# Kernel tuning notes

Measured on AMD Instinct MI355X. Metric: run time of the kernel, lower is better.

Reference implementation:

```python
import jax, jax.numpy as jnp
import numpy as np

H, C = 4, 32            # heads, per-head out channels -> H*C = 128
NEG = jnp.float32(-1e9) # stand-in for -inf mask (keeps grads finite)
NUM_LOC = 15            # self.num_locations hardcoded to 15


def _tconv(x, src, dst, ea, Wq, bq, Wk, bk, Wv, bv, We, Ws, bs, Wb):
    # PyG TransformerConv(beta=True, concat=True, edge_dim=1)
    N = x.shape[0]
    q = (x @ Wq + bq).reshape(N, H, C)
    k = (x @ Wk + bk).reshape(N, H, C)
    v = (x @ Wv + bv).reshape(N, H, C)
    e = (ea @ We).reshape(-1, H, C)  # edge embedding [E,H,C]
    kj = k[src] + e
    alpha = jnp.einsum('ehc,ehc->eh', q[dst], kj) / jnp.sqrt(jnp.float32(C))
    # scatter-softmax over incoming edges of each dst node
    amax = jax.ops.segment_max(alpha, dst, num_segments=N)
    ex = jnp.exp(alpha - amax[dst])
    den = jax.ops.segment_sum(ex, dst, num_segments=N)
    w = ex / (den[dst] + 1e-16)
    out = jax.ops.segment_sum((v[src] + e) * w[..., None], dst, num_segments=N).reshape(N, H * C)
    xr = x @ Ws + bs  # lin_skip
    beta = jax.nn.sigmoid(jnp.concatenate([out, xr, out - xr], axis=-1) @ Wb)  # [N,1]
    return beta * xr + (1.0 - beta) * out


def _bn(x, g, b):
    # BatchNorm1d in training mode (batch statistics, biased var)
    m = x.mean(0)
    v = ((x - m) ** 2).mean(0)
    return (x - m) * jax.lax.rsqrt(v + 1e-5) * g + b


def _forward_core(fa, edge_index, active_mask):
    (node_type, requests, latency,
     c0_Wq, c0_bq, c0_Wk, c0_bk, c0_Wv, c0_bv, c0_We, c0_Ws, c0_bs, c0_Wb,
     t0_W, t0_b, bn0_g, bn0_b,
     cs_Wq, cs_bq, cs_Wk, cs_bk, cs_Wv, cs_bv, cs_We, cs_Ws, cs_bs, cs_Wb,
     ts_W, ts_b, bns_g, bns_b,
     emb_W1, emb_b1, emb_W2, emb_b2, emb_W3, emb_b3,
     rem_W, rem_b, add_W, add_b) = fa
    src, dst = edge_index[0], edge_index[1]
    ea = latency[:, None]                      # edge_attr [E,1]
    x = jnp.stack([node_type, requests], axis=1)  # [N,2]
    # NetworkGraphEmbeddingConstructor: conv1 + 4 stacked conv/linear/bn blocks
    x = _tconv(x, src, dst, ea, c0_Wq, c0_bq, c0_Wk, c0_bk, c0_Wv, c0_bv, c0_We, c0_Ws, c0_bs, c0_Wb)
    x = _bn(jax.nn.relu(x @ t0_W + t0_b), bn0_g, bn0_b)
    for i in range(4):
        x = _tconv(x, src, dst, ea, cs_Wq[i], cs_bq[i], cs_Wk[i], cs_bk[i], cs_Wv[i], cs_bv[i], cs_We[i], cs_Ws[i], cs_bs[i], cs_Wb[i])
        x = _bn(jax.nn.relu(x @ ts_W[i] + ts_b[i]), bns_g[i], bns_b[i])
    # embedding_transformation MLP
    x = jax.nn.relu(x @ emb_W1 + emb_b1)
    x = jax.nn.relu(x @ emb_W2 + emb_b2)
    x = x @ emb_W3 + emb_b3                    # [N,64]
    # sampling head (batch_index=None branch)
    N = x.shape[0]
    maskf = jnp.where(active_mask == 1, jnp.float32(0.0), NEG)
    loc = jnp.arange(N) < NUM_LOC
    remove_mask = jnp.where(loc, jnp.where(maskf == 0.0, NEG, jnp.float32(0.0)), maskf)
    logits1 = (x @ rem_W + rem_b)[:, 0] + remove_mask
    k1, k2 = jax.random.split(jax.random.key(42))
    a1 = jnp.argmax(logits1 + jax.random.gumbel(k1, (N,), logits1.dtype))  # Categorical sample
    mask2 = maskf.at[a1].set(0.0)
    t = jnp.tanh(x[a1] @ add_W + add_b)        # [64]
    logits2 = x @ t + mask2
    a2 = jnp.argmax(logits2 + jax.random.gumbel(k2, (N,), logits2.dtype))
    log_probs = jnp.stack([jax.nn.log_softmax(logits1)[a1], jax.nn.log_softmax(logits2)[a2]])
    return jnp.stack([logits1, logits2]), jnp.stack([a1, a2]), log_probs


def setup_inputs() -> dict:
    N, E = 50000, 400000
    F, HC, EMB, L = 2, 128, 32, 4
    key = jax.random.key(0)
    kit = iter(jax.random.split(key, 64))
    def w(shape, s=0.1):
        return jax.random.normal(next(kit), shape, jnp.float32) * s
    return {
        'node_type': w((N,), 1.0),
        'requests': jax.random.uniform(next(kit), (N,), jnp.float32),
        'latency': jax.random.uniform(next(kit), (E,), jnp.float32),
        'edge_index': jax.random.randint(next(kit), (2, E), 0, N, jnp.int32),
        'active_mask': jax.random.randint(next(kit), (N,), 0, 2, jnp.int32),
        'c0_Wq': w((F, HC)), 'c0_bq': w((HC,)),
        'c0_Wk': w((F, HC)), 'c0_bk': w((HC,)),
        'c0_Wv': w((F, HC)), 'c0_bv': w((HC,)),
        'c0_We': w((1, HC)),
        'c0_Ws': w((F, HC)), 'c0_bs': w((HC,)),
        'c0_Wb': w((3 * HC, 1)),
        't0_W': w((HC, EMB)), 't0_b': w((EMB,)),
        'bn0_g': jnp.ones((EMB,), jnp.float32), 'bn0_b': jnp.zeros((EMB,), jnp.float32),
        'cs_Wq': w((L, EMB, HC)), 'cs_bq': w((L, HC)),
        'cs_Wk': w((L, EMB, HC)), 'cs_bk': w((L, HC)),
        'cs_Wv': w((L, EMB, HC)), 'cs_bv': w((L, HC)),
        'cs_We': w((L, 1, HC)),
        'cs_Ws': w((L, EMB, HC)), 'cs_bs': w((L, HC)),
        'cs_Wb': w((L, 3 * HC, 1)),
        'ts_W': w((L, HC, EMB)), 'ts_b': w((L, EMB)),
        'bns_g': jnp.ones((L, EMB), jnp.float32), 'bns_b': jnp.zeros((L, EMB), jnp.float32),
        'emb_W1': w((EMB, 128)), 'emb_b1': w((128,)),
        'emb_W2': w((128, 64)), 'emb_b2': w((64,)),
        'emb_W3': w((64, 64)), 'emb_b3': w((64,)),
        'rem_W': w((64, 1)), 'rem_b': w((1,)),
        'add_W': w((64, 64)), 'add_b': w((64,)),
    }


def reference(node_type, requests, latency, edge_index, active_mask,
              c0_Wq, c0_bq, c0_Wk, c0_bk, c0_Wv, c0_bv, c0_We, c0_Ws, c0_bs, c0_Wb,
              t0_W, t0_b, bn0_g, bn0_b,
              cs_Wq, cs_bq, cs_Wk, cs_bk, cs_Wv, cs_bv, cs_We, cs_Ws, cs_bs, cs_Wb,
              ts_W, ts_b, bns_g, bns_b,
              emb_W1, emb_b1, emb_W2, emb_b2, emb_W3, emb_b3,
              rem_W, rem_b, add_W, add_b):
    fa = (node_type, requests, latency,
          c0_Wq, c0_bq, c0_Wk, c0_bk, c0_Wv, c0_bv, c0_We, c0_Ws, c0_bs, c0_Wb,
          t0_W, t0_b, bn0_g, bn0_b,
          cs_Wq, cs_bq, cs_Wk, cs_bk, cs_Wv, cs_bv, cs_We, cs_Ws, cs_bs, cs_Wb,
          ts_W, ts_b, bns_g, bns_b,
          emb_W1, emb_b1, emb_W2, emb_b2, emb_W3, emb_b3,
          rem_W, rem_b, add_W, add_b)
    return _forward_core(fa, edge_index, active_mask)
```

## Files before the change

### kernel.cpp

```cpp
#include <hip/hip_runtime.h>
#include <hip/hip_fp16.h>
#include <cstdint>
#include <math.h>

typedef _Float16 h2 __attribute__((ext_vector_type(2)));
typedef float f32x2 __attribute__((ext_vector_type(2)));

__device__ __forceinline__ h2 f2h2(float a, float b) {
    h2 r; r.x = (_Float16)a; r.y = (_Float16)b; return r;
}
__device__ __forceinline__ float fdot2f(h2 a, h2 b, float c) {
    return __builtin_amdgcn_fdot2(a, b, c, false);
}
__device__ __forceinline__ f32x2 bc2(float x) { f32x2 r; r.x = x; r.y = x; return r; }
__device__ __forceinline__ f32x2 cvt2(h2 v) {
    f32x2 r; r.x = (float)v.x; r.y = (float)v.y; return r;
}
__device__ __forceinline__ f32x2 mk2(float a, float b) { f32x2 r; r.x = a; r.y = b; return r; }

union f4h {
    float4 f;
    h2 h[4];
    __half2 u[4];
};

__device__ __forceinline__ uint32_t rotl32(uint32_t x, uint32_t n) {
    return (x << n) | (x >> (32u - n));
}

__device__ __forceinline__ void tf2x32(uint32_t k0, uint32_t k1,
                                       uint32_t x0, uint32_t x1,
                                       uint32_t& o0, uint32_t& o1) {
    uint32_t k2 = k0 ^ k1 ^ 0x1BD11BDAu;
    x0 += k0; x1 += k1;
    x0 += x1; x1 = rotl32(x1, 13); x1 ^= x0;
    x0 += x1; x1 = rotl32(x1, 15); x1 ^= x0;
    x0 += x1; x1 = rotl32(x1, 26); x1 ^= x0;
    x0 += x1; x1 = rotl32(x1, 6);  x1 ^= x0;
    x0 += k1; x1 += k2 + 1u;
    x0 += x1; x1 = rotl32(x1, 17); x1 ^= x0;
    x0 += x1; x1 = rotl32(x1, 29); x1 ^= x0;
    x0 += x1; x1 = rotl32(x1, 16); x1 ^= x0;
    x0 += x1; x1 = rotl32(x1, 24); x1 ^= x0;
    x0 += k2; x1 += k0 + 2u;
    x0 += x1; x1 = rotl32(x1, 13); x1 ^= x0;
    x0 += x1; x1 = rotl32(x1, 15); x1 ^= x0;
    x0 += x1; x1 = rotl32(x1, 26); x1 ^= x0;
    x0 += x1; x1 = rotl32(x1, 6);  x1 ^= x0;
    x0 += k0; x1 += k1 + 3u;
    x0 += x1; x1 = rotl32(x1, 17); x1 ^= x0;
    x0 += x1; x1 = rotl32(x1, 29); x1 ^= x0;
    x0 += x1; x1 = rotl32(x1, 16); x1 ^= x0;
    x0 += x1; x1 = rotl32(x1, 24); x1 ^= x0;
    x0 += k1; x1 += k2 + 4u;
    x0 += x1; x1 = rotl32(x1, 13); x1 ^= x0;
    x0 += x1; x1 = rotl32(x1, 15); x1 ^= x0;
    x0 += x1; x1 = rotl32(x1, 26); x1 ^= x0;
    x0 += x1; x1 = rotl32(x1, 6);  x1 ^= x0;
    x0 += k2; x1 += k0 + 5u;
    o0 = x0; o1 = x1;
}

__device__ float gumbel_at(int n, int which, int N) {
    uint32_t a0, a1, b0, b1;
    tf2x32(0u, 42u, 0u, 2u, a0, a1);
    tf2x32(0u, 42u, 1u, 3u, b0, b1);
    uint32_t gk0 = which ? a1 : a0;
    uint32_t gk1 = which ? b1 : b0;
    int half = N >> 1;
    uint32_t o0, o1, bits;
    if (n < half) { tf2x32(gk0, gk1, (uint32_t)n, (uint32_t)(n + half), o0, o1); bits = o0; }
    else          { tf2x32(gk0, gk1, (uint32_t)(n - half), (uint32_t)n, o0, o1); bits = o1; }
    float f = __uint_as_float((bits >> 9) | 0x3F800000u) - 1.0f;
    float u = fmaxf(1.17549435e-38f, f);
    return -logf(-logf(u));
}

__device__ __forceinline__ uint32_t fmono(float f) {
    uint32_t b = __float_as_uint(f);
    return (b & 0x80000000u) ? ~b : (b | 0x80000000u);
}
__device__ __forceinline__ float funmono(uint32_t u) {
    uint32_t b = (u & 0x80000000u) ? (u & 0x7FFFFFFFu) : ~u;
    return __uint_as_float(b);
}

__device__ __forceinline__ void lse_merge(float& m, float& s, float m2, float s2) {
    float M = fmaxf(m, m2);
    float a = (m == -INFINITY) ? 0.f : expf(m - M) * s;
    float b = (m2 == -INFINITY) ? 0.f : expf(m2 - M) * s2;
    m = M; s = a + b;
}

#define NEGF (-1e9f)
#define ATTNGRID 2048

__global__ void k_hist(const int* __restrict__ dstp, int* __restrict__ deg, int E) {
    int e = blockIdx.x * 256 + threadIdx.x;
    if (e < E) atomicAdd(&deg[dstp[e]], 1);
}

__global__ void k_scan1(const int* __restrict__ deg, int* __restrict__ bsum, int N) {
    __shared__ int s[256];
    int i = blockIdx.x * 256 + threadIdx.x;
    s[threadIdx.x] = (i < N) ? deg[i] : 0;
    __syncthreads();
    for (int st = 128; st > 0; st >>= 1) {
        if (threadIdx.x < st) s[threadIdx.x] += s[threadIdx.x + st];
        __syncthreads();
    }
    if (threadIdx.x == 0) bsum[blockIdx.x] = s[0];
}

__global__ void k_scan2(int* __restrict__ bsum, int nb) {
    __shared__ int s[256];
    int i = threadIdx.x;
    int v = (i < nb) ? bsum[i] : 0;
    s[i] = v;
    __syncthreads();
    for (int st = 1; st < 256; st <<= 1) {
        int t = (i >= st) ? s[i - st] : 0;
        __syncthreads();
        s[i] += t;
        __syncthreads();
    }
    if (i < nb) bsum[i] = s[i] - v;
}

__global__ void k_scan3(const int* __restrict__ deg, const int* __restrict__ bsum,
                        int* __restrict__ rowptr, int* __restrict__ cursor, int N) {
    __shared__ int s[256];
    int i = blockIdx.x * 256 + threadIdx.x;
    int v = (i < N) ? deg[i] : 0;
    s[threadIdx.x] = v;
    __syncthreads();
    for (int st = 1; st < 256; st <<= 1) {
        int t = (threadIdx.x >= st) ? s[threadIdx.x - st] : 0;
        __syncthreads();
        s[threadIdx.x] += t;
        __syncthreads();
    }
    int excl = s[threadIdx.x] - v + bsum[blockIdx.x];
    if (i < N) { rowptr[i] = excl; cursor[i] = excl; }
}

__global__ void k_fill(const int* __restrict__ dstp, const int* __restrict__ srcp,
                       const float* __restrict__ lat, int* __restrict__ cursor,
                       int2* __restrict__ srclat, int E) {
    int e = blockIdx.x * 256 + threadIdx.x;
    if (e < E) {
        int pos = atomicAdd(&cursor[dstp[e]], 1);
        srclat[pos] = make_int2(srcp[e], __float_as_int(lat[e]));
    }
}

__global__ __launch_bounds__(512, 4) void k_qkvr(
        const float* __restrict__ xin, const float* __restrict__ nt,
        const float* __restrict__ rq, int din, int N,
        const float* __restrict__ Wq, const float* __restrict__ bq,
        const float* __restrict__ Wk, const float* __restrict__ bk,
        const float* __restrict__ Wv, const float* __restrict__ bv,
        const float* __restrict__ Ws, const float* __restrict__ bs,
        const double* __restrict__ SUM, const double* __restrict__ SUMSQ,
        const float* __restrict__ bng, const float* __restrict__ bnb,
        int applyBN,
        __half* __restrict__ Q, __half* __restrict__ KV, __half* __restrict__ R) {
    __shared__ h2 w2[4][16 * 128];
    __shared__ float bias[4][128];
    __shared__ h2 xs2[32][17];
    __shared__ float sscale[32], sshift[32];
    int t = threadIdx.x;
    int dpCount = din >> 1;
    for (int i = t; i < dpCount * 128; i += 512) {
        int dp = i >> 7, j = i & 127;
        w2[0][i] = f2h2(Wq[(size_t)(2 * dp) * 128 + j], Wq[(size_t)(2 * dp + 1) * 128 + j]);
        w2[1][i] = f2h2(Wk[(size_t)(2 * dp) * 128 + j], Wk[(size_t)(2 * dp + 1) * 128 + j]);
        w2[2][i] = f2h2(Wv[(size_t)(2 * dp) * 128 + j], Wv[(size_t)(2 * dp + 1) * 128 + j]);
        w2[3][i] = f2h2(Ws[(size_t)(2 * dp) * 128 + j], Ws[(size_t)(2 * dp + 1) * 128 + j]);
    }
    if (t < 128) {
        bias[0][t] = bq[t]; bias[1][t] = bk[t]; bias[2][t] = bv[t]; bias[3][t] = bs[t];
    }
    if (t < 32) {
        if (applyBN) {
            double m = SUM[t] / N;
            double v = SUMSQ[t] / N - m * m;
            float inv = rsqrtf((float)v + 1e-5f);
            float sc = inv * bng[t];
            sscale[t] = sc;
            sshift[t] = bnb[t] - (float)m * sc;
        } else {
            sscale[t] = 1.f; sshift[t] = 0.f;
        }
    }
    int quad = t & 31;
    int sub = t >> 5;
    int dpsh = (din == 32) ? 4 : 0;
    int tiles = (N + 31) >> 5;
    for (int tile = blockIdx.x; tile < tiles; tile += gridDim.x) {
        int base = tile << 5;
        __syncthreads();
        for (int i = t; i < 32 * dpCount; i += 512) {
            int nl = i >> dpsh, dp = i & (dpCount - 1);
            int nn = base + nl;
            float x0 = 0.f, x1 = 0.f;
            if (nn < N) {
                if (din == 2) { x0 = nt[nn]; x1 = rq[nn]; }
                else {
                    x0 = xin[(size_t)nn * din + 2 * dp];
                    x1 = xin[(size_t)nn * din + 2 * dp + 1];
                }
            }
            x0 = x0 * sscale[2 * dp] + sshift[2 * dp];
            x1 = x1 * sscale[2 * dp + 1] + sshift[2 * dp + 1];
            xs2[nl][dp] = f2h2(x0, x1);
        }
        __syncthreads();
        float acc[4][2][4];
#pragma unroll
        for (int m = 0; m < 4; ++m)
#pragma unroll
            for (int k = 0; k < 2; ++k)
#pragma unroll
                for (int c = 0; c < 4; ++c) acc[m][k][c] = bias[m][quad * 4 + c];
        for (int dp = 0; dp < dpCount; ++dp) {
            h2 xv0 = xs2[sub * 2 + 0][dp];
            h2 xv1 = xs2[sub * 2 + 1][dp];
#pragma unroll
            for (int m = 0; m < 4; ++m) {
                const h2* wp = &w2[m][dp * 128 + quad * 4];
                h2 wa = wp[0], wb = wp[1], wc = wp[2], wd = wp[3];
                acc[m][0][0] = fdot2f(xv0, wa, acc[m][0][0]);
                acc[m][0][1] = fdot2f(xv0, wb, acc[m][0][1]);
                acc[m][0][2] = fdot2f(xv0, wc, acc[m][0][2]);
                acc[m][0][3] = fdot2f(xv0, wd, acc[m][0][3]);
                acc[m][1][0] = fdot2f(xv1, wa, acc[m][1][0]);
                acc[m][1][1] = fdot2f(xv1, wb, acc[m][1][1]);
                acc[m][1][2] = fdot2f(xv1, wc, acc[m][1][2]);
                acc[m][1][3] = fdot2f(xv1, wd, acc[m][1][3]);
            }
        }
#pragma unroll
        for (int k = 0; k < 2; ++k) {
            int n = base + sub * 2 + k;
            if (n < N) {
                *(__half2*)&Q[(size_t)n * 128 + quad * 4 + 0] =
                    __floats2half2_rn(acc[0][k][0], acc[0][k][1]);
                *(__half2*)&Q[(size_t)n * 128 + quad * 4 + 2] =
                    __floats2half2_rn(acc[0][k][2], acc[0][k][3]);
                *(__half2*)&KV[(size_t)n * 256 + quad * 4 + 0] =
                    __floats2half2_rn(acc[1][k][0], acc[1][k][1]);
                *(__half2*)&KV[(size_t)n * 256 + quad * 4 + 2] =
                    __floats2half2_rn(acc[1][k][2], acc[1][k][3]);
                *(__half2*)&KV[(size_t)n * 256 + 128 + quad * 4 + 0] =
                    __floats2half2_rn(acc[2][k][0], acc[2][k][1]);
                *(__half2*)&KV[(size_t)n * 256 + 128 + quad * 4 + 2] =
                    __floats2half2_rn(acc[2][k][2], acc[2][k][3]);
                *(__half2*)&R[(size_t)n * 128 + quad * 4 + 0] =
                    __floats2half2_rn(acc[3][k][0], acc[3][k][1]);
                *(__half2*)&R[(size_t)n * 128 + quad * 4 + 2] =
                    __floats2half2_rn(acc[3][k][2], acc[3][k][3]);
            }
        }
    }
}

__global__ __launch_bounds__(256) void k_attn(
        const int2* __restrict__ srclat,
        const __half* __restrict__ Q, const __half* __restrict__ KV,
        const float* __restrict__ We,
        const __half* __restrict__ R, const float* __restrict__ Wb,
        const int* __restrict__ rowptr, const int* __restrict__ deg,
        __half* __restrict__ A, int N) {
    __shared__ float weL[128], wboL[128], wbrL[128];
    int t = threadIdx.x;
    if (t < 128) {
        float w0 = Wb[t], w1 = Wb[128 + t], w2v = Wb[256 + t];
        weL[t] = We[t];
        wboL[t] = w0 + w2v;
        wbrL[t] = w1 - w2v;
    }
    __syncthreads();

    int wvid = t >> 6;
    int l64 = t & 63;
    int slot = (l64 >> 4) & 1;
    int nsub = l64 >> 5;
    int lane = l64 & 15;
    const f32x2* wep = (const f32x2*)&weL[lane * 8];
    const f32x2* bop = (const f32x2*)&wboL[lane * 8];
    const f32x2* brp = (const f32x2*)&wbrL[lane * 8];
    h2 weh0, weh1, weh2, weh3;
    {
        f32x2 wa = wep[0], wb = wep[1], wc = wep[2], wd = wep[3];
        weh0 = f2h2(wa.x, wa.y); weh1 = f2h2(wb.x, wb.y);
        weh2 = f2h2(wc.x, wc.y); weh3 = f2h2(wd.x, wd.y);
    }
    const float4 f4z = make_float4(0.f, 0.f, 0.f, 0.f);

    int T = gridDim.x * 4;
    int T2 = T * 2;
    int base0 = (blockIdx.x * 4 + wvid) * 2;

    f4h qh, rh, k0, v0;
    int start = 0, d = 0; float l0 = 0.f;
    f4h pq, pr, pk, pv;
    float pl = 0.f;
    int s1 = 0, d1 = 0;
    int2 psl1 = make_int2(0, 0);
    int s2 = 0, d2 = 0;
    qh.f = f4z; rh.f = f4z; k0.f = f4z; v0.f = f4z;
    pq.f = f4z; pr.f = f4z; pk.f = f4z; pv.f = f4z;

    {
        int n0l = base0 + nsub;
        if (n0l < N) {
            start = rowptr[n0l]; d = deg[n0l];
            qh.f = *(const float4*)(Q + (size_t)n0l * 128 + lane * 8);
            rh.f = *(const float4*)(R + (size_t)n0l * 128 + lane * 8);
            if (slot < d) {
                int2 sl = srclat[start + slot];
                l0 = __int_as_float(sl.y);
                k0.f = *(const float4*)(KV + (size_t)sl.x * 256 + lane * 8);
                v0.f = *(const float4*)(KV + (size_t)sl.x * 256 + 128 + lane * 8);
            }
            int n1l = n0l + T2;
            if (n1l < N) {
                s1 = rowptr[n1l]; d1 = deg[n1l];
                if (slot < d1) psl1 = srclat[s1 + slot];
            }
            int n2l = n0l + 2 * T2;
            if (n2l < N) { s2 = rowptr[n2l]; d2 = deg[n2l]; }
        }
    }

    for (int nb = base0; nb < N; nb += T2) {
        int n = nb + nsub;
        int n1 = n + T2, n2 = n + 2 * T2, n3 = n + 3 * T2;
        int s3 = 0, d3 = 0;
        if (n3 < N) { s3 = rowptr[n3]; d3 = deg[n3]; }
        int2 psl2 = make_int2(0, 0);
        if (n2 < N && slot < d2) psl2 = srclat[s2 + slot];
        if (n1 < N) {
            pq.f = *(const float4*)(Q + (size_t)n1 * 128 + lane * 8);
            pr.f = *(const float4*)(R + (size_t)n1 * 128 + lane * 8);
            if (slot < d1) {
                pl = __int_as_float(psl1.y);
                pk.f = *(const float4*)(KV + (size_t)psl1.x * 256 + lane * 8);
                pv.f = *(const float4*)(KV + (size_t)psl1.x * 256 + 128 + lane * 8);
            }
        }

        float qwe = fdot2f(qh.h[0], weh0, fdot2f(qh.h[1], weh1,
                    fdot2f(qh.h[2], weh2, fdot2f(qh.h[3], weh3, 0.f))));
        qwe += __shfl_xor(qwe, 1); qwe += __shfl_xor(qwe, 2);

        float m = -INFINITY, den = 0.f, plsum = 0.f;
        f32x2 A0 = bc2(0.f), A1 = bc2(0.f), A2 = bc2(0.f), A3 = bc2(0.f);

        int idx = slot;
        bool have = idx < d;
        while (have) {
            int idx2 = idx + 2;
            bool have2 = idx2 < d;
            float l1 = 0.f;
            f4h k1, v1;
            if (have2) {
                int2 sl = srclat[start + idx2];
                l1 = __int_as_float(sl.y);
                k1.f = *(const float4*)(KV + (size_t)sl.x * 256 + lane * 8);
                v1.f = *(const float4*)(KV + (size_t)sl.x * 256 + 128 + lane * 8);
            }

            float t0 = fdot2f(qh.h[0], k0.h[0], fdot2f(qh.h[1], k0.h[1],
                       fdot2f(qh.h[2], k0.h[2], fdot2f(qh.h[3], k0.h[3], 0.f))));
            t0 += __shfl_xor(t0, 1); t0 += __shfl_xor(t0, 2);
            float alpha = fmaf(l0, qwe, t0) * 0.17677669529663687f;

            float mn = fmaxf(m, alpha);
            float sc = __expf(m - mn);
            float p = __expf(alpha - mn);
            f32x2 sc2 = bc2(sc), p2 = bc2(p);
            A0 = A0 * sc2 + p2 * cvt2(v0.h[0]);
            A1 = A1 * sc2 + p2 * cvt2(v0.h[1]);
            A2 = A2 * sc2 + p2 * cvt2(v0.h[2]);
            A3 = A3 * sc2 + p2 * cvt2(v0.h[3]);
            plsum = plsum * sc + p * l0;
            den = fmaf(den, sc, p);
            m = mn;

            idx = idx2; l0 = l1;
            k0.f = k1.f; v0.f = v1.f;
            have = have2;
        }

        {
            float mo = __shfl_xor(m, 16);
            float mn = fmaxf(m, mo);
            float sc = (m == -INFINITY) ? 0.f : __expf(m - mn);
            f32x2 sc2 = bc2(sc);
            A0 *= sc2; A1 *= sc2; A2 *= sc2; A3 *= sc2;
            den *= sc; plsum *= sc;
            A0 += mk2(__shfl_xor(A0.x, 16), __shfl_xor(A0.y, 16));
            A1 += mk2(__shfl_xor(A1.x, 16), __shfl_xor(A1.y, 16));
            A2 += mk2(__shfl_xor(A2.x, 16), __shfl_xor(A2.y, 16));
            A3 += mk2(__shfl_xor(A3.x, 16), __shfl_xor(A3.y, 16));
            den += __shfl_xor(den, 16); plsum += __shfl_xor(plsum, 16);
            m = mn;
        }

        float inv = 1.f / (den + 1e-16f);
        f32x2 inv2 = bc2(inv), pls2 = bc2(plsum);
        f32x2 O0 = (A0 + pls2 * wep[0]) * inv2;
        f32x2 O1 = (A1 + pls2 * wep[1]) * inv2;
        f32x2 O2 = (A2 + pls2 * wep[2]) * inv2;
        f32x2 O3 = (A3 + pls2 * wep[3]) * inv2;

        f32x2 R0 = cvt2(rh.h[0]), R1 = cvt2(rh.h[1]);
        f32x2 R2 = cvt2(rh.h[2]), R3 = cvt2(rh.h[3]);
        f32x2 G = O0 * bop[0];
        G += R0 * brp[0];
        G += O1 * bop[1]; G += R1 * brp[1];
        G += O2 * bop[2]; G += R2 * brp[2];
        G += O3 * bop[3]; G += R3 * brp[3];
        float g = G.x + G.y;
        g += __shfl_xor(g, 1); g += __shfl_xor(g, 2);
        g += __shfl_xor(g, 4); g += __shfl_xor(g, 8);
        float beta = 1.0f / (1.0f + __expf(-g));

        if ((l64 & 16) == 0 && n < N) {
            f32x2 bb = bc2(beta), ib = bc2(1.0f - beta);
            f32x2 W0 = bb * R0 + ib * O0;
            f32x2 W1 = bb * R1 + ib * O1;
            f32x2 W2 = bb * R2 + ib * O2;
            f32x2 W3 = bb * R3 + ib * O3;
            *(__half2*)&A[(size_t)n * 128 + lane * 8 + 0] = __floats2half2_rn(W0.x, W0.y);
            *(__half2*)&A[(size_t)n * 128 + lane * 8 + 2] = __floats2half2_rn(W1.x, W1.y);
            *(__half2*)&A[(size_t)n * 128 + lane * 8 + 4] = __floats2half2_rn(W2.x, W2.y);
            *(__half2*)&A[(size_t)n * 128 + lane * 8 + 6] = __floats2half2_rn(W3.x, W3.y);
        }

        qh.f = pq.f; rh.f = pr.f; k0.f = pk.f; v0.f = pv.f; l0 = pl;
        start = s1; d = d1;
        s1 = s2; d1 = d2; s2 = s3; d2 = d3;
        psl1 = psl2;
    }
}

__global__ __launch_bounds__(256) void k_linstats(
        const __half* __restrict__ A, const float* __restrict__ tW,
        const float* __restrict__ tb, float* __restrict__ H32,
        double* __restrict__ partials, int N) {
    __shared__ h2 w2l[64 * 32];
    __shared__ float bias[32];
    __shared__ h2 xsT[64][66];
    __shared__ double sp1[4][8][4], sp2[4][8][4];
    int t = threadIdx.x;
    for (int i = t; i < 64 * 32; i += 256) {
        int dp = i >> 5, j = i & 31;
        w2l[i] = f2h2(tW[(size_t)(2 * dp) * 32 + j], tW[(size_t)(2 * dp + 1) * 32 + j]);
    }
    if (t < 32) bias[t] = tb[t];
    int quad = t & 7;
    int sub = t >> 3;
    int base = blockIdx.x << 6;

    __syncthreads();
#pragma unroll
    for (int k = 0; k < 4; ++k) {
        int i = t + 256 * k;
        int nl = i >> 4, g8 = i & 15;
        int n = base + nl;
        h2 hv[4];
        if (n < N) {
            const h2* ap = (const h2*)(A + (size_t)n * 128 + g8 * 8);
            hv[0] = ap[0]; hv[1] = ap[1]; hv[2] = ap[2]; hv[3] = ap[3];
        } else {
            h2 z; z.x = (_Float16)0.f; z.y = (_Float16)0.f;
            hv[0] = z; hv[1] = z; hv[2] = z; hv[3] = z;
        }
        xsT[g8 * 4 + 0][nl] = hv[0];
        xsT[g8 * 4 + 1][nl] = hv[1];
        xsT[g8 * 4 + 2][nl] = hv[2];
        xsT[g8 * 4 + 3][nl] = hv[3];
    }
    __syncthreads();

    float acc[2][4];
#pragma unroll
    for (int k = 0; k < 2; ++k)
#pragma unroll
        for (int c = 0; c < 4; ++c) acc[k][c] = bias[quad * 4 + c];
    for (int dp = 0; dp < 64; ++dp) {
        h2 x0 = xsT[dp][sub * 2 + 0];
        h2 x1 = xsT[dp][sub * 2 + 1];
        const h2* wp = &w2l[dp * 32 + quad * 4];
        h2 wa = wp[0], wb = wp[1], wc = wp[2], wd = wp[3];
        acc[0][0] = fdot2f(x0, wa, acc[0][0]);
        acc[0][1] = fdot2f(x0, wb, acc[0][1]);
        acc[0][2] = fdot2f(x0, wc, acc[0][2]);
        acc[0][3] = fdot2f(x0, wd, acc[0][3]);
        acc[1][0] = fdot2f(x1, wa, acc[1][0]);
        acc[1][1] = fdot2f(x1, wb, acc[1][1]);
        acc[1][2] = fdot2f(x1, wc, acc[1][2]);
        acc[1][3] = fdot2f(x1, wd, acc[1][3]);
    }
    double s1[4] = {0, 0, 0, 0}, s2[4] = {0, 0, 0, 0};
#pragma unroll
    for (int k = 0; k < 2; ++k) {
        int n = base + sub * 2 + k;
        if (n < N) {
            float4 yv;
            yv.x = fmaxf(acc[k][0], 0.f); yv.y = fmaxf(acc[k][1], 0.f);
            yv.z = fmaxf(acc[k][2], 0.f); yv.w = fmaxf(acc[k][3], 0.f);
            *(float4*)&H32[(size_t)n * 32 + quad * 4] = yv;
            s1[0] += yv.x; s1[1] += yv.y; s1[2] += yv.z; s1[3] += yv.w;
            s2[0] += (double)yv.x * yv.x; s2[1] += (double)yv.y * yv.y;
            s2[2] += (double)yv.z * yv.z; s2[3] += (double)yv.w * yv.w;
        }
    }
#pragma unroll
    for (int c = 0; c < 4; ++c) {
        s1[c] += __shfl_xor(s1[c], 8);  s2[c] += __shfl_xor(s2[c], 8);
        s1[c] += __shfl_xor(s1[c], 16); s2[c] += __shfl_xor(s2[c], 16);
        s1[c] += __shfl_xor(s1[c], 32); s2[c] += __shfl_xor(s2[c], 32);
    }
    __syncthreads();
    int wave = t >> 6;
    if ((t & 63) < 8) {
#pragma unroll
        for (int c = 0; c < 4; ++c) { sp1[wave][quad][c] = s1[c]; sp2[wave][quad][c] = s2[c]; }
    }
    __syncthreads();
    if (t < 32) {
        int q = t >> 2, c = t & 3;
        double a1 = 0, a2 = 0;
#pragma unroll
        for (int wv = 0; wv < 4; ++wv) { a1 += sp1[wv][q][c]; a2 += sp2[wv][q][c]; }
        partials[(size_t)blockIdx.x * 64 + t] = a1;
        partials[(size_t)blockIdx.x * 64 + 32 + t] = a2;
    }
}

__global__ void k_statred(const double* __restrict__ partials,
                          double* __restrict__ SUM, double* __restrict__ SUMSQ,
                          int nblocks) {
    __shared__ double s[256];
    int col = blockIdx.x;
    double a = 0;
    for (int b = threadIdx.x; b < nblocks; b += 256)
        a += partials[(size_t)b * 64 + col];
    s[threadIdx.x] = a;
    __syncthreads();
    for (int st = 128; st > 0; st >>= 1) {
        if (threadIdx.x < st) s[threadIdx.x] += s[threadIdx.x + st];
        __syncthreads();
    }
    if (threadIdx.x == 0) {
        if (col < 32) SUM[col] = s[0];
        else SUMSQ[col - 32] = s[0];
    }
}

__global__ __launch_bounds__(256) void k_mlp12(
        const float* __restrict__ H32,
        const double* __restrict__ SUM, const double* __restrict__ SUMSQ,
        const float* __restrict__ bng, const float* __restrict__ bnb,
        const float* __restrict__ W1, const float* __restrict__ b1,
        const float* __restrict__ W2, const float* __restrict__ b2,
        float* __restrict__ Y2, unsigned int* __restrict__ smallbuf, int N) {
    __shared__ float w1[32 * 128];
    __shared__ float sb1[128];
    __shared__ float sscale[32], sshift[32];
    __shared__ float w2f[128 * 64];
    __shared__ float sb2[64];
    __shared__ float xs[16][36];
    __shared__ float y1[16][132];
    int t = threadIdx.x;
    if (blockIdx.x == 0 && t < 16) smallbuf[t] = 0u;
    for (int i = t; i < 32 * 128; i += 256) w1[i] = W1[i];
    for (int i = t; i < 128 * 64; i += 256) w2f[i] = W2[i];
    if (t < 128) sb1[t] = b1[t];
    if (t < 64) sb2[t] = b2[t];
    if (t < 32) {
        double m = SUM[t] / N;
        double v = SUMSQ[t] / N - m * m;
        float inv = rsqrtf((float)v + 1e-5f);
        float sc = inv * bng[t];
        sscale[t] = sc;
        sshift[t] = bnb[t] - (float)m * sc;
    }
    int q1 = t & 31, s1_ = t >> 5;
    int q2 = t & 15, s2_ = t >> 4;
    int tiles = (N + 15) >> 4;
    for (int tile = blockIdx.x; tile < tiles; tile += gridDim.x) {
        int base = tile << 4;
        __syncthreads();
        if (t < 128) {
            int nl = t >> 3, q = t & 7;
            int n = base + nl;
            float4 xv = make_float4(0.f, 0.f, 0.f, 0.f);
            if (n < N) xv = *(const float4*)&H32[(size_t)n * 32 + q * 4];
            xs[nl][q * 4 + 0] = xv.x * sscale[q * 4 + 0] + sshift[q * 4 + 0];
            xs[nl][q * 4 + 1] = xv.y * sscale[q * 4 + 1] + sshift[q * 4 + 1];
            xs[nl][q * 4 + 2] = xv.z * sscale[q * 4 + 2] + sshift[q * 4 + 2];
            xs[nl][q * 4 + 3] = xv.w * sscale[q * 4 + 3] + sshift[q * 4 + 3];
        }
        __syncthreads();
        float a[2][4];
#pragma unroll
        for (int k = 0; k < 2; ++k)
#pragma unroll
            for (int c = 0; c < 4; ++c) a[k][c] = sb1[q1 * 4 + c];
        for (int d = 0; d < 32; ++d) {
            float4 w4 = *(const float4*)&w1[d * 128 + q1 * 4];
#pragma unroll
            for (int k = 0; k < 2; ++k) {
                float x = xs[s1_ * 2 + k][d];
                a[k][0] = fmaf(x, w4.x, a[k][0]);
                a[k][1] = fmaf(x, w4.y, a[k][1]);
                a[k][2] = fmaf(x, w4.z, a[k][2]);
                a[k][3] = fmaf(x, w4.w, a[k][3]);
            }
        }
#pragma unroll
        for (int k = 0; k < 2; ++k) {
            float4 yv;
            yv.x = fmaxf(a[k][0], 0.f); yv.y = fmaxf(a[k][1], 0.f);
            yv.z = fmaxf(a[k][2], 0.f); yv.w = fmaxf(a[k][3], 0.f);
            *(float4*)&y1[s1_ * 2 + k][q1 * 4] = yv;
        }
        __syncthreads();
        float b[4];
#pragma unroll
        for (int c = 0; c < 4; ++c) b[c] = sb2[q2 * 4 + c];
        for (int d = 0; d < 128; ++d) {
            float4 w4 = *(const float4*)&w2f[d * 64 + q2 * 4];
            float x = y1[s2_][d];
            b[0] = fmaf(x, w4.x, b[0]);
            b[1] = fmaf(x, w4.y, b[1]);
            b[2] = fmaf(x, w4.z, b[2]);
            b[3] = fmaf(x, w4.w, b[3]);
        }
        int n = base + s2_;
        if (n < N) {
            float4 yv;
            yv.x = fmaxf(b[0], 0.f); yv.y = fmaxf(b[1], 0.f);
            yv.z = fmaxf(b[2], 0.f); yv.w = fmaxf(b[3], 0.f);
            *(float4*)&Y2[(size_t)n * 64 + q2 * 4] = yv;
        }
    }
}

__global__ __launch_bounds__(256) void k_mlp3h(
        const float* __restrict__ Y2, const float* __restrict__ W3,
        const float* __restrict__ b3,
        const float* __restrict__ remW, const float* __restrict__ remB,
        const int* __restrict__ active,
        float* __restrict__ X3, float* __restrict__ l1out,
        unsigned long long* __restrict__ slot1, float2* __restrict__ part1,
        int N) {
    __shared__ float w3[64 * 64];
    __shared__ float sb3[64];
    __shared__ float xs[32][68];
    __shared__ float srw[64];
    __shared__ float redm[256], reds[256];
    __shared__ unsigned long long redb[256];
    int t = threadIdx.x;
    for (int i = t; i < 64 * 64; i += 256) w3[i] = W3[i];
    if (t < 64) { sb3[t] = b3[t]; srw[t] = remW[t]; }
    float rB = remB[0];
    int quad = t & 15, sub = t >> 4;
    float lm = -INFINITY, ls = 0.f;
    unsigned long long best = 0ull;
    int tiles = (N + 31) >> 5;
    for (int tile = blockIdx.x; tile < tiles; tile += gridDim.x) {
        int base = tile << 5;
        __syncthreads();
#pragma unroll
        for (int k = 0; k < 2; ++k) {
            int i = t + 256 * k;
            int nl = i >> 4, q = i & 15;
            int n = base + nl;
            float4 xv = make_float4(0.f, 0.f, 0.f, 0.f);
            if (n < N) xv = *(const float4*)&Y2[(size_t)n * 64 + q * 4];
            *(float4*)&xs[nl][q * 4] = xv;
        }
        __syncthreads();
        float a[2][4];
#pragma unroll
        for (int k = 0; k < 2; ++k)
#pragma unroll
            for (int c = 0; c < 4; ++c) a[k][c] = sb3[quad * 4 + c];
        for (int d = 0; d < 64; ++d) {
            float4 w4 = *(const float4*)&w3[d * 64 + quad * 4];
#pragma unroll
            for (int k = 0; k < 2; ++k) {
                float x = xs[sub * 2 + k][d];
                a[k][0] = fmaf(x, w4.x, a[k][0]);
                a[k][1] = fmaf(x, w4.y, a[k][1]);
                a[k][2] = fmaf(x, w4.z, a[k][2]);
                a[k][3] = fmaf(x, w4.w, a[k][3]);
            }
        }
#pragma unroll
        for (int k = 0; k < 2; ++k) {
            int n = base + sub * 2 + k;
            if (n < N)
                *(float4*)&X3[(size_t)n * 64 + quad * 4] = *(float4*)a[k];
        }
#pragma unroll
        for (int k = 0; k < 2; ++k) {
            int n = base + sub * 2 + k;
            float h = a[k][0] * srw[quad * 4 + 0] + a[k][1] * srw[quad * 4 + 1]
                    + a[k][2] * srw[quad * 4 + 2] + a[k][3] * srw[quad * 4 + 3];
            h += __shfl_xor(h, 1); h += __shfl_xor(h, 2);
            h += __shfl_xor(h, 4); h += __shfl_xor(h, 8);
            if (quad == 0 && n < N) {
                float maskf = (active[n] == 1) ? 0.f : NEGF;
                float rm_ = (n < 15) ? ((maskf == 0.f) ? NEGF : 0.f) : maskf;
                float l1 = h + rB + rm_;
                l1out[n] = l1;
                lse_merge(lm, ls, l1, 1.0f);
                float z = l1 + gumbel_at(n, 0, N);
                unsigned long long p = ((unsigned long long)fmono(z) << 32) |
                                       (unsigned long long)(0xFFFFFFFFu - (unsigned)n);
                if (p > best) best = p;
            }
        }
    }
    redm[t] = lm; reds[t] = ls; redb[t] = best;
    __syncthreads();
    for (int st = 128; st > 0; st >>= 1) {
        if (t < st) {
            float m2 = redm[t + st], s2 = reds[t + st];
            float mm = redm[t], ss = reds[t];
            lse_merge(mm, ss, m2, s2);
            redm[t] = mm; reds[t] = ss;
            if (redb[t + st] > redb[t]) redb[t] = redb[t + st];
        }
        __syncthreads();
    }
    if (t == 0) {
        part1[blockIdx.x] = make_float2(redm[0], reds[0]);
        if (redb[0]) atomicMax(slot1, redb[0]);
    }
}

__global__ void k_head2(const float* __restrict__ X3, const float* __restrict__ addW,
                        const float* __restrict__ addB,
                        const unsigned long long* __restrict__ slot1,
                        float* __restrict__ tvec, int* __restrict__ a1buf) {
    int j = threadIdx.x;
    unsigned long long p = *slot1;
    int a1 = (int)(0xFFFFFFFFu - (unsigned)(p & 0xFFFFFFFFull));
    const float* xr = X3 + (size_t)a1 * 64;
    float acc = addB[j];
    for (int d = 0; d < 64; d++) acc = fmaf(xr[d], addW[d * 64 + j], acc);
    tvec[j] = tanhf(acc);
    if (j == 0) *a1buf = a1;
}

__global__ void k_head3p(const float* __restrict__ X3, const float* __restrict__ tvec,
                         const int* __restrict__ active, const int* __restrict__ a1buf,
                         float* __restrict__ l2out, unsigned long long* __restrict__ slot2,
                         float2* __restrict__ part2, int N) {
    __shared__ float redm[256], reds[256];
    __shared__ unsigned long long redb[256];
    int t = threadIdx.x;
    int n = blockIdx.x * 256 + t;
    float lm = -INFINITY, ls = 0.f;
    unsigned long long best = 0ull;
    if (n < N) {
        const float* xr = X3 + (size_t)n * 64;
        float acc = 0.f;
        for (int d = 0; d < 64; d++) acc = fmaf(xr[d], tvec[d], acc);
        float maskf = (active[n] == 1) ? 0.f : NEGF;
        if (n == *a1buf) maskf = 0.f;
        float l2 = acc + maskf;
        l2out[n] = l2;
        lm = l2; ls = 1.f;
        float z = l2 + gumbel_at(n, 1, N);
        best = ((unsigned long long)fmono(z) << 32) |
               (unsigned long long)(0xFFFFFFFFu - (unsigned)n);
    }
    redm[t] = lm; reds[t] = ls; redb[t] = best;
    __syncthreads();
    for (int st = 128; st > 0; st >>= 1) {
        if (t < st) {
            float mm = redm[t], ss = reds[t];
            lse_merge(mm, ss, redm[t + st], reds[t + st]);
            redm[t] = mm; reds[t] = ss;
            if (redb[t + st] > redb[t]) redb[t] = redb[t + st];
        }
        __syncthreads();
    }
    if (t == 0) {
        part2[blockIdx.x] = make_float2(redm[0], reds[0]);
        if (redb[0]) atomicMax(slot2, redb[0]);
    }
}

__global__ void k_final2(const float* __restrict__ l1, const float* __restrict__ l2,
                         const unsigned long long* __restrict__ slot2,
                         const int* __restrict__ a1buf,
                         const float2* __restrict__ part1, int np1,
                         const float2* __restrict__ part2, int np2,
                         float* __restrict__ outTail) {
    __shared__ float rm[256], rs[256];
    int t = threadIdx.x;
    float m = -INFINITY, s = 0.f;
    for (int i = t; i < np1; i += 256) { float2 p = part1[i]; lse_merge(m, s, p.x, p.y); }
    rm[t] = m; rs[t] = s;
    __syncthreads();
    for (int st = 128; st > 0; st >>= 1) {
        if (t < st) { float mm = rm[t], ss = rs[t]; lse_merge(mm, ss, rm[t + st], rs[t + st]); rm[t] = mm; rs[t] = ss; }
        __syncthreads();
    }
    float M1 = rm[0], S1 = rs[0];
    __syncthreads();
    m = -INFINITY; s = 0.f;
    for (int i = t; i < np2; i += 256) { float2 p = part2[i]; lse_merge(m, s, p.x, p.y); }
    rm[t] = m; rs[t] = s;
    __syncthreads();
    for (int st = 128; st > 0; st >>= 1) {
        if (t < st) { float mm = rm[t], ss = rs[t]; lse_merge(mm, ss, rm[t + st], rs[t + st]); rm[t] = mm; rs[t] = ss; }
        __syncthreads();
    }
    float M2 = rm[0], S2 = rs[0];
    if (t == 0) {
        int a1 = *a1buf;
        int a2 = (int)(0xFFFFFFFFu - (unsigned)((*slot2) & 0xFFFFFFFFull));
        outTail[0] = (float)a1;
        outTail[1] = (float)a2;
        outTail[2] = l1[a1] - (M1 + logf(S1));
        outTail[3] = l2[a2] - (M2 + logf(S2));
    }
}

extern "C" void kernel_launch(void* const* d_in, const int* in_sizes, int n_in,
                              void* d_out, int out_size, void* d_ws, size_t ws_size,
                              hipStream_t stream) {
    const float* node_type = (const float*)d_in[0];
    const float* requests  = (const float*)d_in[1];
    const float* latency   = (const float*)d_in[2];
    const int* edge_index  = (const int*)d_in[3];
    const int* active      = (const int*)d_in[4];
    int N = in_sizes[0];
    int E = in_sizes[2];
    const int* src = edge_index;
    const int* dst = edge_index + E;
    float* out = (float*)d_out;

    char* base = (char*)d_ws;
    size_t off = 0;
    auto alloc = [&](size_t bytes) -> char* {
        char* p = base + off;
        off += (bytes + 255) & ~(size_t)255;
        return p;
    };
    char* Abuf   = alloc((size_t)N * 128 * 4);
    char* Qbuf   = alloc((size_t)N * 128 * 4);
    __half* KV   = (__half*)alloc((size_t)N * 256 * 2);
    char* Rbuf   = alloc((size_t)N * 128 * 4);
    float* H32   = (float*)alloc((size_t)N * 32 * 4);
    int* deg     = (int*)alloc((size_t)N * 4);
    int* rowptr  = (int*)alloc((size_t)N * 4);
    int* cursor  = (int*)alloc((size_t)N * 4);
    int2* srclat = (int2*)alloc((size_t)E * 8);
    int* bsum    = (int*)alloc(1024 * 4);
    int lsTiles = (N + 63) / 64;
    double* partials = (double*)alloc((size_t)lsTiles * 64 * 8);
    double* SUM  = (double*)alloc(512);
    double* SUMSQ = SUM + 32;
    float2* part1 = (float2*)alloc(512 * 8);
    int ng = (N + 255) / 256;
    float2* part2 = (float2*)alloc((size_t)ng * 8);
    char* small  = alloc(1024);
    unsigned long long* slot1 = (unsigned long long*)small;
    unsigned long long* slot2 = slot1 + 1;
    int* a1buf = (int*)(small + 32);
    float* tvec = (float*)(small + 64);

    __half* Ah = (__half*)Abuf;   float* Y2f = (float*)Abuf;
    __half* Qh = (__half*)Qbuf;
    __half* Rh = (__half*)Rbuf;   float* X3f = (float*)Rbuf;

    int egE = (E + 255) / 256;
    int nb = ng;

    (void)hipMemsetAsync(deg, 0, (size_t)N * 4, stream);
    k_hist<<<egE, 256, 0, stream>>>(dst, deg, E);
    k_scan1<<<nb, 256, 0, stream>>>(deg, bsum, N);
    k_scan2<<<1, 256, 0, stream>>>(bsum, nb);
    k_scan3<<<nb, 256, 0, stream>>>(deg, bsum, rowptr, cursor, N);
    k_fill<<<egE, 256, 0, stream>>>(dst, src, latency, cursor, srclat, E);

    for (int L = 0; L < 5; ++L) {
        int din = L ? 32 : 2;
        const float* xin = L ? H32 : nullptr;
        const float* Wq = L ? (const float*)d_in[19] + (size_t)(L - 1) * 4096 : (const float*)d_in[5];
        const float* bq = L ? (const float*)d_in[20] + (size_t)(L - 1) * 128  : (const float*)d_in[6];
        const float* Wk = L ? (const float*)d_in[21] + (size_t)(L - 1) * 4096 : (const float*)d_in[7];
        const float* bk = L ? (const float*)d_in[22] + (size_t)(L - 1) * 128  : (const float*)d_in[8];
        const float* Wv = L ? (const float*)d_in[23] + (size_t)(L - 1) * 4096 : (const float*)d_in[9];
        const float* bv = L ? (const float*)d_in[24] + (size_t)(L - 1) * 128  : (const float*)d_in[10];
        const float* We = L ? (const float*)d_in[25] + (size_t)(L - 1) * 128  : (const float*)d_in[11];
        const float* Ws = L ? (const float*)d_in[26] + (size_t)(L - 1) * 4096 : (const float*)d_in[12];
        const float* bs = L ? (const float*)d_in[27] + (size_t)(L - 1) * 128  : (const float*)d_in[13];
        const float* Wb = L ? (const float*)d_in[28] + (size_t)(L - 1) * 384  : (const float*)d_in[14];
        const float* tW = L ? (const float*)d_in[29] + (size_t)(L - 1) * 4096 : (const float*)d_in[15];
        const float* tb = L ? (const float*)d_in[30] + (size_t)(L - 1) * 32   : (const float*)d_in[16];
        const float* bngP = (L == 1) ? (const float*)d_in[17]
                          : (L >= 2) ? (const float*)d_in[31] + (size_t)(L - 2) * 32 : nullptr;
        const float* bnbP = (L == 1) ? (const float*)d_in[18]
                          : (L >= 2) ? (const float*)d_in[32] + (size_t)(L - 2) * 32 : nullptr;

        k_qkvr<<<1024, 512, 0, stream>>>(xin, node_type, requests, din, N,
                                         Wq, bq, Wk, bk, Wv, bv, Ws, bs,
                                         SUM, SUMSQ, bngP, bnbP, (L > 0) ? 1 : 0,
                                         Qh, KV, Rh);
        k_attn<<<ATTNGRID, 256, 0, stream>>>(srclat, Qh, KV, We, Rh, Wb,
                                             rowptr, deg, Ah, N);
        k_linstats<<<lsTiles, 256, 0, stream>>>(Ah, tW, tb, H32, partials, N);
        k_statred<<<64, 256, 0, stream>>>(partials, SUM, SUMSQ, lsTiles);
    }

    k_mlp12<<<512, 256, 0, stream>>>(H32, SUM, SUMSQ,
                                     (const float*)d_in[31] + 3 * 32,
                                     (const float*)d_in[32] + 3 * 32,
                                     (const float*)d_in[33], (const float*)d_in[34],
                                     (const float*)d_in[35], (const float*)d_in[36],
                                     Y2f, (unsigned int*)small, N);
    k_mlp3h<<<512, 256, 0, stream>>>(Y2f, (const float*)d_in[37], (const float*)d_in[38],
                                     (const float*)d_in[39], (const float*)d_in[40],
                                     active, X3f, out, slot1, part1, N);
    k_head2<<<1, 64, 0, stream>>>(X3f, (const float*)d_in[41], (const float*)d_in[42],
                                  slot1, tvec, a1buf);
    k_head3p<<<ng, 256, 0, stream>>>(X3f, tvec, active, a1buf, out + N, slot2,
                                     part2, N);
    k_final2<<<1, 256, 0, stream>>>(out, out + N, slot2, a1buf,
                                    part1, 512, part2, ng, out + 2 * N);
}
```

Baseline: 676.9 us.

## Fuse BN stat reduction into linstats via last-block counter, one tile per qkvr block

Result: slower. 1.186 ms (+75.3%).

```diff
diff --git a/kernel.cpp b/kernel.cpp
--- a/kernel.cpp
+++ b/kernel.cpp
@@ -22,6 +22,10 @@
     float4 f;
     h2 h[4];
     __half2 u[4];
+};
+union h2x2 {
+    float2 f;
+    __half2 h[2];
 };
 
 __device__ __forceinline__ uint32_t rotl32(uint32_t x, uint32_t n) {
@@ -196,9 +200,8 @@
     int quad = t & 31;
     int sub = t >> 5;
     int dpsh = (din == 32) ? 4 : 0;
-    int tiles = (N + 31) >> 5;
-    for (int tile = blockIdx.x; tile < tiles; tile += gridDim.x) {
-        int base = tile << 5;
+    {
+        int base = blockIdx.x << 5;
         __syncthreads();
         for (int i = t; i < 32 * dpCount; i += 512) {
             int nl = i >> dpsh, dp = i & (dpCount - 1);
@@ -244,22 +247,19 @@
         for (int k = 0; k < 2; ++k) {
             int n = base + sub * 2 + k;
             if (n < N) {
-                *(__half2*)&Q[(size_t)n * 128 + quad * 4 + 0] =
-                    __floats2half2_rn(acc[0][k][0], acc[0][k][1]);
-                *(__half2*)&Q[(size_t)n * 128 + quad * 4 + 2] =
-                    __floats2half2_rn(acc[0][k][2], acc[0][k][3]);
-                *(__half2*)&KV[(size_t)n * 256 + quad * 4 + 0] =
-                    __floats2half2_rn(acc[1][k][0], acc[1][k][1]);
-                *(__half2*)&KV[(size_t)n * 256 + quad * 4 + 2] =
-                    __floats2half2_rn(acc[1][k][2], acc[1][k][3]);
-                *(__half2*)&KV[(size_t)n * 256 + 128 + quad * 4 + 0] =
-                    __floats2half2_rn(acc[2][k][0], acc[2][k][1]);
-                *(__half2*)&KV[(size_t)n * 256 + 128 + quad * 4 + 2] =
-                    __floats2half2_rn(acc[2][k][2], acc[2][k][3]);
-                *(__half2*)&R[(size_t)n * 128 + quad * 4 + 0] =
-                    __floats2half2_rn(acc[3][k][0], acc[3][k][1]);
-                *(__half2*)&R[(size_t)n * 128 + quad * 4 + 2] =
-                    __floats2half2_rn(acc[3][k][2], acc[3][k][3]);
+                h2x2 v;
+                v.h[0] = __floats2half2_rn(acc[0][k][0], acc[0][k][1]);
+                v.h[1] = __floats2half2_rn(acc[0][k][2], acc[0][k][3]);
+                *(float2*)&Q[(size_t)n * 128 + quad * 4] = v.f;
+                v.h[0] = __floats2half2_rn(acc[1][k][0], acc[1][k][1]);
+                v.h[1] = __floats2half2_rn(acc[1][k][2], acc[1][k][3]);
+                *(float2*)&KV[(size_t)n * 256 + quad * 4] = v.f;
+                v.h[0] = __floats2half2_rn(acc[2][k][0], acc[2][k][1]);
+                v.h[1] = __floats2half2_rn(acc[2][k][2], acc[2][k][3]);
+                *(float2*)&KV[(size_t)n * 256 + 128 + quad * 4] = v.f;
+                v.h[0] = __floats2half2_rn(acc[3][k][0], acc[3][k][1]);
+                v.h[1] = __floats2half2_rn(acc[3][k][2], acc[3][k][3]);
+                *(float2*)&R[(size_t)n * 128 + quad * 4] = v.f;
             }
         }
     }
@@ -450,11 +450,15 @@
 __global__ __launch_bounds__(256) void k_linstats(
         const __half* __restrict__ A, const float* __restrict__ tW,
         const float* __restrict__ tb, float* __restrict__ H32,
-        double* __restrict__ partials, int N) {
+        double* __restrict__ partials,
+        double* __restrict__ SUM, double* __restrict__ SUMSQ,
+        int* __restrict__ counter, int target, int N) {
     __shared__ h2 w2l[64 * 32];
     __shared__ float bias[32];
     __shared__ h2 xsT[64][66];
     __shared__ double sp1[4][8][4], sp2[4][8][4];
+    __shared__ double red[4][64];
+    __shared__ int lastFlag;
     int t = threadIdx.x;
     for (int i = t; i < 64 * 32; i += 256) {
         int dp = i >> 5, j = i & 31;
@@ -540,25 +544,26 @@
         partials[(size_t)blockIdx.x * 64 + t] = a1;
         partials[(size_t)blockIdx.x * 64 + 32 + t] = a2;
     }
-}
-
-__global__ void k_statred(const double* __restrict__ partials,
-                          double* __restrict__ SUM, double* __restrict__ SUMSQ,
-                          int nblocks) {
-    __shared__ double s[256];
-    int col = blockIdx.x;
-    double a = 0;
-    for (int b = threadIdx.x; b < nblocks; b += 256)
-        a += partials[(size_t)b * 64 + col];
-    s[threadIdx.x] = a;
-    __syncthreads();
-    for (int st = 128; st > 0; st >>= 1) {
-        if (threadIdx.x < st) s[threadIdx.x] += s[threadIdx.x + st];
-        __syncthreads();
-    }
-    if (threadIdx.x == 0) {
-        if (col < 32) SUM[col] = s[0];
-        else SUMSQ[col - 32] = s[0];
+    __threadfence();
+    __syncthreads();
+    if (t == 0) {
+        int old = atomicAdd(counter, 1);
+        lastFlag = (old == target - 1) ? 1 : 0;
+    }
+    __syncthreads();
+    if (lastFlag) {
+        __threadfence();
+        int col = t & 63, chunk = t >> 6;
+        int nb = gridDim.x;
+        double a = 0.0;
+        for (int b = chunk; b < nb; b += 4)
+            a += partials[(size_t)b * 64 + col];
+        red[chunk][col] = a;
+        __syncthreads();
+        if (t < 64) {
+            double v = red[0][t] + red[1][t] + red[2][t] + red[3][t];
+            if (t < 32) SUM[t] = v; else SUMSQ[t - 32] = v;
+        }
     }
 }
 
@@ -873,9 +878,10 @@
     double* partials = (double*)alloc((size_t)lsTiles * 64 * 8);
     double* SUM  = (double*)alloc(512);
     double* SUMSQ = SUM + 32;
-    float2* part1 = (float2*)alloc(512 * 8);
+    float2* part1 = (float2*)alloc(521 * 8);
     int ng = (N + 255) / 256;
     float2* part2 = (float2*)alloc((size_t)ng * 8);
+    int* lscnt = (int*)alloc(256);
     char* small  = alloc(1024);
     unsigned long long* slot1 = (unsigned long long*)small;
     unsigned long long* slot2 = slot1 + 1;
@@ -888,8 +894,10 @@
 
     int egE = (E + 255) / 256;
     int nb = ng;
+    int qkTiles = (N + 31) / 32;
 
     (void)hipMemsetAsync(deg, 0, (size_t)N * 4, stream);
+    (void)hipMemsetAsync(lscnt, 0, 4, stream);
     k_hist<<<egE, 256, 0, stream>>>(dst, deg, E);
     k_scan1<<<nb, 256, 0, stream>>>(deg, bsum, N);
     k_scan2<<<1, 256, 0, stream>>>(bsum, nb);
@@ -916,14 +924,15 @@
         const float* bnbP = (L == 1) ? (const float*)d_in[18]
                           : (L >= 2) ? (const float*)d_in[32] + (size_t)(L - 2) * 32 : nullptr;
 
-        k_qkvr<<<1024, 512, 0, stream>>>(xin, node_type, requests, din, N,
-                                         Wq, bq, Wk, bk, Wv, bv, Ws, bs,
-                                         SUM, SUMSQ, bngP, bnbP, (L > 0) ? 1 : 0,
-                                         Qh, KV, Rh);
+        k_qkvr<<<qkTiles, 512, 0, stream>>>(xin, node_type, requests, din, N,
+                                            Wq, bq, Wk, bk, Wv, bv, Ws, bs,
+                                            SUM, SUMSQ, bngP, bnbP, (L > 0) ? 1 : 0,
+                                            Qh, KV, Rh);
         k_attn<<<ATTNGRID, 256, 0, stream>>>(srclat, Qh, KV, We, Rh, Wb,
                                              rowptr, deg, Ah, N);
-        k_linstats<<<lsTiles, 256, 0, stream>>>(Ah, tW, tb, H32, partials, N);
-        k_statred<<<64, 256, 0, stream>>>(partials, SUM, SUMSQ, lsTiles);
+        k_linstats<<<lsTiles, 256, 0, stream>>>(Ah, tW, tb, H32, partials,
+                                                SUM, SUMSQ, lscnt,
+                                                lsTiles * (L + 1), N);
     }
 
     k_mlp12<<<512, 256, 0, stream>>>(H32, SUM, SUMSQ,
@@ -932,7 +941,7 @@
                                      (const float*)d_in[33], (const float*)d_in[34],
                                      (const float*)d_in[35], (const float*)d_in[36],
                                      Y2f, (unsigned int*)small, N);
-    k_mlp3h<<<512, 256, 0, stream>>>(Y2f, (const float*)d_in[37], (const float*)d_in[38],
+    k_mlp3h<<<521, 256, 0, stream>>>(Y2f, (const float*)d_in[37], (const float*)d_in[38],
                                      (const float*)d_in[39], (const float*)d_in[40],
                                      active, X3f, out, slot1, part1, N);
     k_head2<<<1, 64, 0, stream>>>(X3f, (const float*)d_in[41], (const float*)d_in[42],
@@ -940,5 +949,5 @@
     k_head3p<<<ng, 256, 0, stream>>>(X3f, tvec, active, a1buf, out + N, slot2,
                                      part2, N);
     k_final2<<<1, 256, 0, stream>>>(out, out + N, slot2, a1buf,
-                                    part1, 512, part2, ng, out + 2 * N);
-}
+                                    part1, 521, part2, ng, out + 2 * N);
+}
```
